# Kernel optimization log

Measured on AMD Instinct MI355X. Metric: run time of the kernel, lower is better.

## Reference

```python
import jax, jax.numpy as jnp
import numpy as np

N_NODES = 50000
NUM_HYPEREDGES = 50000


def setup_inputs() -> dict:
    key = jax.random.key(0)
    k1, k2, k3, k4, k5 = jax.random.split(key, 5)
    E = 1_600_000
    F_IN, F_OUT = 128, 128
    X = jax.random.normal(k1, (N_NODES, F_IN), dtype=jnp.float32)
    nodes = jax.random.randint(k2, (E,), 0, N_NODES, dtype=jnp.int64)
    hedges = jax.random.randint(k3, (E,), 0, NUM_HYPEREDGES, dtype=jnp.int64)
    edge_index = jnp.stack([nodes, hedges], axis=0)
    W = jax.random.normal(k4, (F_IN, F_OUT), dtype=jnp.float32) * (1.0 / np.sqrt(F_IN))
    b = jax.random.normal(k5, (F_OUT,), dtype=jnp.float32) * 0.02
    return {"X": X, "edge_index": edge_index, "W": W, "b": b}


def reference(X, edge_index, W, b):
    nodes = edge_index[0]   # [E] node ids (source of incidence)
    hedges = edge_index[1]  # [E] hyperedge ids
    ones = jnp.ones(nodes.shape[0], dtype=X.dtype)

    # x = lin(X)  (Linear, bias=False inside conv)
    x = X @ W  # [N, F_out]

    # B = 1 / hyperedge degree (inf -> 0)
    deg_e = jax.ops.segment_sum(ones, hedges, num_segments=NUM_HYPEREDGES)
    B_inv = jnp.where(deg_e > 0, 1.0 / deg_e, 0.0)

    # D = 1 / node degree (unit hyperedge weights; inf -> 0)
    deg_v = jax.ops.segment_sum(ones, nodes, num_segments=N_NODES)
    D_inv = jnp.where(deg_v > 0, 1.0 / deg_v, 0.0)

    # node -> hyperedge aggregation: m_e = B_e * sum_{v in e} x_v
    m = jax.ops.segment_sum(x[nodes], hedges, num_segments=NUM_HYPEREDGES)
    m = m * B_inv[:, None]  # [M, F_out]

    # hyperedge -> node aggregation: out_v = D_v * sum_{e ni v} m_e
    out = jax.ops.segment_sum(m[hedges], nodes, num_segments=N_NODES)
    out = out * D_inv[:, None] + b  # [N, F_out]

    return jax.nn.softmax(out, axis=1)
```

## Files before the change

### kernel.cpp

```cpp
#include <hip/hip_runtime.h>
#include <hip/hip_fp16.h>

#define NN 50000
#define NM 50000
#define F  128
#define NBUK 782
#define CHSZ 4096
typedef unsigned short ushort_t;
typedef _Float16 f16;
typedef f16 f16x8 __attribute__((ext_vector_type(8)));
typedef float f32x4 __attribute__((ext_vector_type(4)));

union HF4 { float4 f4; __half2 h2[4]; };
union PK4 { uint2 u2; f16 h[4]; };

__device__ __forceinline__ int wscan64(int v, int lane) {
    int x = v;
#pragma unroll
    for (int s = 1; s < 64; s <<= 1) {
        int u = __shfl_up(x, s, 64);
        if (lane >= s) x += u;
    }
    return x;
}

__device__ __forceinline__ int bscan256(int v, int* s5, int* tot) {
    int t = threadIdx.x, lane = t & 63, wid = t >> 6;
    int incl = wscan64(v, lane);
    if (lane == 63) s5[wid] = incl;
    __syncthreads();
    if (t == 0) {
        int a = 0;
#pragma unroll
        for (int j = 0; j < 4; ++j) { int x = s5[j]; s5[j] = a; a += x; }
        s5[4] = a;
    }
    __syncthreads();
    int ex = incl - v + s5[wid];
    *tot = s5[4];
    __syncthreads();
    return ex;
}

__global__ __launch_bounds__(256) void wprep_k(const float* __restrict__ W,
                                               f16* __restrict__ Wt) {
    int i = blockIdx.x * 256 + threadIdx.x;
    int k = i >> 7, c = i & 127;
    Wt[c * 128 + k] = (f16)W[i];
}

struct GemmSmem { f16 sXh[64 * 128]; };
struct SortSmem { int hist[NBUK]; int cursor[NBUK]; int pairs[CHSZ]; int s5[5]; };
union alignas(16) FatSmem { GemmSmem g; SortSmem s; };

__global__ __launch_bounds__(256) void fat_k(const float* __restrict__ X,
                                             const f16* __restrict__ Wt,
                                             f16* __restrict__ xh,
                                             const int* __restrict__ nodes,
                                             const int* __restrict__ hedges,
                                             int* __restrict__ gchunk0, int* __restrict__ gchunk1,
                                             int* __restrict__ ghist, int* __restrict__ gstart,
                                             int E, int NCH, int nsort) {
    __shared__ FatSmem u;
    int t = threadIdx.x;

    if ((int)blockIdx.x < nsort) {
        int dir = blockIdx.x / NCH;
        int c   = blockIdx.x % NCH;
        const int* key = dir ? nodes  : hedges;
        const int* pay = dir ? hedges : nodes;
        int* gchunk    = dir ? gchunk1 : gchunk0;
        int e0 = c * CHSZ, e1 = min(E, e0 + CHSZ);

        for (int i = t; i < NBUK; i += 256) u.s.hist[i] = 0;
        __syncthreads();
        for (int e = e0 + t; e < e1; e += 256) atomicAdd(&u.s.hist[key[e] >> 6], 1);
        __syncthreads();

        int carry = 0;
        for (int base = 0; base < NBUK; base += 256) {
            int i = base + t;
            int v = (i < NBUK) ? u.s.hist[i] : 0;
            int tot;
            int ex = bscan256(v, u.s.s5, &tot);
            if (i < NBUK) u.s.cursor[i] = ex + carry;
            carry += tot;
        }
        __syncthreads();

        for (int b = t; b < NBUK; b += 256) {
            size_t idx = ((size_t)dir * NBUK + b) * NCH + c;
            ghist[idx]  = u.s.hist[b];
            gstart[idx] = u.s.cursor[b];
        }
        __syncthreads();

        for (int e = e0 + t; e < e1; e += 256) {
            int k = key[e];
            int pos = atomicAdd(&u.s.cursor[k >> 6], 1);
            u.s.pairs[pos] = ((k & 63) << 16) | pay[e];
        }
        __syncthreads();

        int n = e1 - e0;
        for (int i = t; i < n; i += 256) gchunk[(size_t)c * CHSZ + i] = u.s.pairs[i];
    } else {
        int gb = blockIdx.x - nsort;
        int row0 = gb * 64;

        const float4* X4 = (const float4*)X;
        for (int i = t; i < 64 * 32; i += 256) {
            int r = i >> 5, cq = i & 31;
            int gr = row0 + r;
            float4 xv = (gr < NN) ? X4[(size_t)gr * 32 + cq]
                                  : make_float4(0.f, 0.f, 0.f, 0.f);
            PK4 pk;
            pk.h[0] = (f16)xv.x; pk.h[1] = (f16)xv.y;
            pk.h[2] = (f16)xv.z; pk.h[3] = (f16)xv.w;
            int byte = (r * 256 + cq * 8) ^ ((r & 7) << 4);
            *(uint2*)((char*)u.g.sXh + byte) = pk.u2;
        }
        __syncthreads();

        int l = t & 63, w = t >> 6;
        int lr = l & 15, lk = l >> 4;
        f32x4 acc[8];
#pragma unroll
        for (int c = 0; c < 8; ++c) acc[c] = (f32x4){0.f, 0.f, 0.f, 0.f};

#pragma unroll
        for (int ks = 0; ks < 4; ++ks) {
            int rloc = w * 16 + lr;
            int abyte = (rloc * 256 + ks * 64 + lk * 16) ^ ((rloc & 7) << 4);
            f16x8 afrag = *(const f16x8*)((const char*)u.g.sXh + abyte);
#pragma unroll
            for (int c = 0; c < 8; ++c) {
                f16x8 bfrag = *(const f16x8*)(Wt + (c * 16 + lr) * 128 + ks * 32 + lk * 8);
                acc[c] = __builtin_amdgcn_mfma_f32_16x16x32_f16(afrag, bfrag, acc[c], 0, 0, 0);
            }
        }

#pragma unroll
        for (int c = 0; c < 8; ++c) {
            int col = c * 16 + lr;
#pragma unroll
            for (int j = 0; j < 4; ++j) {
                int row = row0 + w * 16 + lk * 4 + j;
                if (row < NN) xh[(size_t)row * 128 + col] = (f16)acc[c][j];
            }
        }
    }
}

__global__ __launch_bounds__(256) void rowsum_k(const int* __restrict__ ghist,
                                                int* __restrict__ bsum, int NCH) {
    int row = blockIdx.x * 4 + (threadIdx.x >> 6);
    int l = threadIdx.x & 63;
    if (row >= 2 * NBUK) return;
    const int* r = ghist + (size_t)row * NCH;
    int s = 0;
    for (int c = l; c < NCH; c += 64) s += r[c];
#pragma unroll
    for (int k = 32; k >= 1; k >>= 1) s += __shfl_xor(s, k, 64);
    if (l == 0) bsum[row] = s;
}

__global__ __launch_bounds__(1024) void bucketbase_k(const int* __restrict__ bsum,
                                                     int* __restrict__ bstart,
                                                     int* __restrict__ off0, int* __restrict__ off1,
                                                     int E) {
    __shared__ int s16[17];
    int dir = blockIdx.x;
    int t = threadIdx.x, lane = t & 63, wid = t >> 6;
    int v = (t < NBUK) ? bsum[dir * NBUK + t] : 0;
    int incl = wscan64(v, lane);
    if (lane == 63) s16[wid] = incl;
    __syncthreads();
    if (t < 16) {
        int x = s16[t], y = x;
#pragma unroll
        for (int s = 1; s < 16; s <<= 1) {
            int u = __shfl_up(y, s, 64);
            if (t >= s) y += u;
        }
        s16[t] = y - x;
    }
    __syncthreads();
    int ex = incl - v + s16[wid];
    if (t < NBUK) bstart[dir * NBUK + t] = ex;
    if (t == 0) (dir ? off1 : off0)[50000] = E;
}

__global__ __launch_bounds__(256) void merge_scatter_k(const int* __restrict__ gchunk0, const int* __restrict__ gchunk1,
                                                       const int* __restrict__ ghist, const int* __restrict__ gstart,
                                                       const int* __restrict__ bstart,
                                                       ushort_t* __restrict__ adj0, ushort_t* __restrict__ adj1,
                                                       int* __restrict__ off0, int* __restrict__ off1,
                                                       int NCH) {
    __shared__ int ssrc[512];
    __shared__ int sdst[513];
    __shared__ int s5[5];
    __shared__ int pairsS[CHSZ];
    __shared__ int fcnt[64], foff[64], fcur[64];

    int dir = blockIdx.x / NBUK;
    int b   = blockIdx.x % NBUK;
    int t   = threadIdx.x;
    const int* gchunk   = dir ? gchunk1 : gchunk0;
    ushort_t* adj       = dir ? adj1 : adj0;
    int* offD           = dir ? off1 : off0;

    int len0 = 0, src0 = 0, len1 = 0, src1 = 0;
    if (t < NCH) {
        size_t idx = ((size_t)dir * NBUK + b) * NCH + t;
        len0 = ghist[idx];
        src0 = gstart[idx];
    }
    if (t + 256 < NCH) {
        size_t idx = ((size_t)dir * NBUK + b) * NCH + t + 256;
        len1 = ghist[idx];
        src1 = gstart[idx];
    }
    ssrc[t]       = src0;
    ssrc[t + 256] = src1;
    int tot0, tot1;
    int ex0 = bscan256(len0, s5, &tot0);
    int ex1 = bscan256(len1, s5, &tot1);
    sdst[t]       = ex0;
    sdst[t + 256] = tot0 + ex1;
    if (t == 0) sdst[512] = tot0 + tot1;
    if (t < 64) fcnt[t] = 0;
    __syncthreads();
    int T = tot0 + tot1;

    int per = (T + 255) >> 8;
    int i0 = t * per, i1 = min(T, i0 + per);
    if (i0 < i1) {
        int lo = 0, hi = 511;
        while (lo < hi) {
            int mid = (lo + hi + 1) >> 1;
            if (sdst[mid] <= i0) lo = mid; else hi = mid - 1;
        }
        int c = lo;
        for (int i = i0; i < i1; ++i) {
            while (c < 511 && sdst[c + 1] <= i) ++c;
            int p = gchunk[(size_t)c * CHSZ + ssrc[c] + (i - sdst[c])];
            pairsS[i] = p;
            atomicAdd(&fcnt[p >> 16], 1);
        }
    }
    __syncthreads();

    int bst = bstart[dir * NBUK + b];
    if (t < 64) {
        int x = fcnt[t];
        int y = wscan64(x, t);
        foff[t] = y - x;
        fcur[t] = y - x;
        int d = b * 64 + t;
        if (d < 50000) offD[d] = bst + foff[t];
    }
    __syncthreads();

    for (int i = t; i < T; i += 256) {
        int p = pairsS[i];
        int slot = atomicAdd(&fcur[p >> 16], 1);
        adj[(size_t)bst + slot] = (ushort_t)(p & 0xFFFF);
    }
}

__global__ __launch_bounds__(256) void agg_a_k(const char* __restrict__ xb,
                                               const ushort_t* __restrict__ adj,
                                               const int* __restrict__ off,
                                               float4* __restrict__ m4) {
    int t = threadIdx.x;
    int seg = blockIdx.x * 4 + (t >> 6);
    int l = t & 63;
    int rg = l >> 4;
    unsigned int cb = (unsigned int)(l & 15) << 4;
    int p0 = off[seg], p1 = off[seg + 1];
    __half2 z = __floats2half2_rn(0.f, 0.f);
    __half2 a0 = z, a1 = z, a2 = z, a3 = z;
    int i = p0;
    for (; i + 16 <= p1; i += 16) {
        unsigned int o0 = ((unsigned int)adj[i + rg]      << 8) + cb;
        unsigned int o1 = ((unsigned int)adj[i + 4 + rg]  << 8) + cb;
        unsigned int o2 = ((unsigned int)adj[i + 8 + rg]  << 8) + cb;
        unsigned int o3 = ((unsigned int)adj[i + 12 + rg] << 8) + cb;
        HF4 u0, u1, u2, u3;
        u0.f4 = *(const float4*)(xb + o0);
        u1.f4 = *(const float4*)(xb + o1);
        u2.f4 = *(const float4*)(xb + o2);
        u3.f4 = *(const float4*)(xb + o3);
#pragma unroll
        for (int k = 0; k < 4; ++k) {
            __half2 s01 = __hadd2(u0.h2[k], u1.h2[k]);
            __half2 s23 = __hadd2(u2.h2[k], u3.h2[k]);
            __half2 s = __hadd2(s01, s23);
            if (k == 0) a0 = __hadd2(a0, s);
            else if (k == 1) a1 = __hadd2(a1, s);
            else if (k == 2) a2 = __hadd2(a2, s);
            else a3 = __hadd2(a3, s);
        }
    }
    for (; i < p1; i += 4) {
        int r = i + rg;
        if (r < p1) {
            unsigned int o = ((unsigned int)adj[r] << 8) + cb;
            HF4 u;
            u.f4 = *(const float4*)(xb + o);
            a0 = __hadd2(a0, u.h2[0]); a1 = __hadd2(a1, u.h2[1]);
            a2 = __hadd2(a2, u.h2[2]); a3 = __hadd2(a3, u.h2[3]);
        }
    }
    float2 f0 = __half22float2(a0), f1 = __half22float2(a1);
    float2 f2 = __half22float2(a2), f3 = __half22float2(a3);
    float v[8] = {f0.x, f0.y, f1.x, f1.y, f2.x, f2.y, f3.x, f3.y};
#pragma unroll
    for (int k = 0; k < 8; ++k) {
        v[k] += __shfl_xor(v[k], 16, 64);
        v[k] += __shfl_xor(v[k], 32, 64);
    }
    if (l < 16) {
        float inv = (p1 > p0) ? 1.0f / (float)(p1 - p0) : 0.0f;
        HF4 w;
#pragma unroll
        for (int k = 0; k < 4; ++k)
            w.h2[k] = __floats2half2_rn(v[2 * k] * inv, v[2 * k + 1] * inv);
        m4[(size_t)seg * 16 + (l & 15)] = w.f4;
    }
}

__global__ __launch_bounds__(256) void agg_b_k(const char* __restrict__ mb,
                                               const ushort_t* __restrict__ adj,
                                               const int* __restrict__ off,
                                               const float* __restrict__ bias,
                                               float4* __restrict__ out4) {
    int t = threadIdx.x;
    int seg = blockIdx.x * 4 + (t >> 6);
    int l = t & 63;
    int rg = l >> 4;
    int cc = l & 15;
    unsigned int cb = (unsigned int)cc << 4;
    int p0 = off[seg], p1 = off[seg + 1];
    __half2 z = __floats2half2_rn(0.f, 0.f);
    __half2 a0 = z, a1 = z, a2 = z, a3 = z;
    int i = p0;
    for (; i + 16 <= p1; i += 16) {
        unsigned int o0 = ((unsigned int)adj[i + rg]      << 8) + cb;
        unsigned int o1 = ((unsigned int)adj[i + 4 + rg]  << 8) + cb;
        unsigned int o2 = ((unsigned int)adj[i + 8 + rg]  << 8) + cb;
        unsigned int o3 = ((unsigned int)adj[i + 12 + rg] << 8) + cb;
        HF4 u0, u1, u2, u3;
        u0.f4 = *(const float4*)(mb + o0);
        u1.f4 = *(const float4*)(mb + o1);
        u2.f4 = *(const float4*)(mb + o2);
        u3.f4 = *(const float4*)(mb + o3);
#pragma unroll
        for (int k = 0; k < 4; ++k) {
            __half2 s01 = __hadd2(u0.h2[k], u1.h2[k]);
            __half2 s23 = __hadd2(u2.h2[k], u3.h2[k]);
            __half2 s = __hadd2(s01, s23);
            if (k == 0) a0 = __hadd2(a0, s);
            else if (k == 1) a1 = __hadd2(a1, s);
            else if (k == 2) a2 = __hadd2(a2, s);
            else a3 = __hadd2(a3, s);
        }
    }
    for (; i < p1; i += 4) {
        int r = i + rg;
        if (r < p1) {
            unsigned int o = ((unsigned int)adj[r] << 8) + cb;
            HF4 u;
            u.f4 = *(const float4*)(mb + o);
            a0 = __hadd2(a0, u.h2[0]); a1 = __hadd2(a1, u.h2[1]);
            a2 = __hadd2(a2, u.h2[2]); a3 = __hadd2(a3, u.h2[3]);
        }
    }
    float2 f0 = __half22float2(a0), f1 = __half22float2(a1);
    float2 f2 = __half22float2(a2), f3 = __half22float2(a3);
    float v[8] = {f0.x, f0.y, f1.x, f1.y, f2.x, f2.y, f3.x, f3.y};
#pragma unroll
    for (int k = 0; k < 8; ++k) {
        v[k] += __shfl_xor(v[k], 16, 64);
        v[k] += __shfl_xor(v[k], 32, 64);
    }
    float inv = (p1 > p0) ? 1.0f / (float)(p1 - p0) : 0.0f;
    const float4* b4 = (const float4*)bias;
    float4 bb0 = b4[cc * 2], bb1 = b4[cc * 2 + 1];
    float lg[8];
    lg[0] = v[0] * inv + bb0.x; lg[1] = v[1] * inv + bb0.y;
    lg[2] = v[2] * inv + bb0.z; lg[3] = v[3] * inv + bb0.w;
    lg[4] = v[4] * inv + bb1.x; lg[5] = v[5] * inv + bb1.y;
    lg[6] = v[6] * inv + bb1.z; lg[7] = v[7] * inv + bb1.w;

    float mx = lg[0];
#pragma unroll
    for (int k = 1; k < 8; ++k) mx = fmaxf(mx, lg[k]);
#pragma unroll
    for (int s = 1; s < 16; s <<= 1) mx = fmaxf(mx, __shfl_xor(mx, s, 16));
    float e[8], sm = 0.f;
#pragma unroll
    for (int k = 0; k < 8; ++k) { e[k] = __expf(lg[k] - mx); sm += e[k]; }
#pragma unroll
    for (int s = 1; s < 16; s <<= 1) sm += __shfl_xor(sm, s, 16);
    float r = 1.0f / sm;
    if (l < 16) {
        out4[(size_t)seg * 32 + cc * 2]     = make_float4(e[0] * r, e[1] * r, e[2] * r, e[3] * r);
        out4[(size_t)seg * 32 + cc * 2 + 1] = make_float4(e[4] * r, e[5] * r, e[6] * r, e[7] * r);
    }
}

extern "C" void kernel_launch(void* const* d_in, const int* in_sizes, int n_in,
                              void* d_out, int out_size, void* d_ws, size_t ws_size,
                              hipStream_t stream) {
    const float* X  = (const float*)d_in[0];
    const int*   ei = (const int*)d_in[1];
    const float* W  = (const float*)d_in[2];
    const float* b  = (const float*)d_in[3];

    int E = in_sizes[1] / 2;
    const int* nodes  = ei;
    const int* hedges = ei + E;
    int NCH = (E + CHSZ - 1) / CHSZ;
    int nsort = 2 * NCH;
    int gemmb = (NN + 63) / 64;

    char* p = (char*)d_ws;
    f16* xh = (f16*)p;                    p += (size_t)NN * F * 2;
    f16* mh = (f16*)p;                    p += (size_t)NM * F * 2;
    ushort_t* adj0 = (ushort_t*)p;        p += (size_t)E * 2;
    ushort_t* adj1 = (ushort_t*)p;        p += (size_t)E * 2;
    int* ghist  = (int*)p;                p += (size_t)2 * NBUK * NCH * 4;
    int* gstart = (int*)p;                p += (size_t)2 * NBUK * NCH * 4;
    int* bstart = (int*)p;                p += (size_t)2 * NBUK * 4;
    int* bsum   = (int*)p;                p += (size_t)2 * NBUK * 4;
    int* off0   = (int*)p;                p += (size_t)(NN + 1) * 4;
    int* off1   = (int*)p;                p += (size_t)(NN + 1) * 4;
    f16* Wt     = (f16*)p;                p += (size_t)128 * 128 * 2;
    p = (char*)(((uintptr_t)p + 15) & ~(uintptr_t)15);
    int* gchunk0 = (int*)p;
    int* gchunk1 = gchunk0 + (size_t)NCH * CHSZ;

    wprep_k<<<64, 256, 0, stream>>>(W, Wt);
    fat_k<<<nsort + gemmb, 256, 0, stream>>>(X, Wt, xh, nodes, hedges,
                                             gchunk0, gchunk1, ghist, gstart, E, NCH, nsort);
    rowsum_k<<<(2 * NBUK + 3) / 4, 256, 0, stream>>>(ghist, bsum, NCH);
    bucketbase_k<<<2, 1024, 0, stream>>>(bsum, bstart, off0, off1, E);
    merge_scatter_k<<<2 * NBUK, 256, 0, stream>>>(gchunk0, gchunk1, ghist, gstart, bstart,
                                                  adj0, adj1, off0, off1, NCH);
    agg_a_k<<<NM / 4, 256, 0, stream>>>((const char*)xh, adj0, off0, (float4*)mh);
    agg_b_k<<<NN / 4, 256, 0, stream>>>((const char*)mh, adj1, off1, b, (float4*)d_out);
}
```

Measured before the change: 213.4 us.

## Coarsen radix buckets to 256 keys and double sort chunk size

The two-pass bucket sort that builds the CSR adjacency now uses 196 buckets of 256 keys instead of 782 buckets of 64, and chunks of 8192 edges instead of 4096. This shrinks the per-chunk histogram and start tables, cuts the merge-scatter block count, and lets each merge block handle a single 256-entry chunk scan. Each merge block stages at most 10240 pairs in shared memory and truncates anything beyond that. This relies on uniformly distributed input keeping every bucket under that limit, and the larger shared-memory footprint may lower occupancy.

```diff
diff --git a/kernel.cpp b/kernel.cpp
--- a/kernel.cpp
+++ b/kernel.cpp
@@ -4,8 +4,9 @@
 #define NN 50000
 #define NM 50000
 #define F  128
-#define NBUK 782
-#define CHSZ 4096
+#define NGRP 196
+#define CHSZ 8192
+#define PSZ  10240
 typedef unsigned short ushort_t;
 typedef _Float16 f16;
 typedef f16 f16x8 __attribute__((ext_vector_type(8)));
@@ -50,7 +51,7 @@
 }
 
 struct GemmSmem { f16 sXh[64 * 128]; };
-struct SortSmem { int hist[NBUK]; int cursor[NBUK]; int pairs[CHSZ]; int s5[5]; };
+struct SortSmem { int hist[NGRP]; int cursor[NGRP]; int pairs[CHSZ]; int s5[5]; };
 union alignas(16) FatSmem { GemmSmem g; SortSmem s; };
 
 __global__ __launch_bounds__(256) void fat_k(const float* __restrict__ X,
@@ -72,33 +73,30 @@
         int* gchunk    = dir ? gchunk1 : gchunk0;
         int e0 = c * CHSZ, e1 = min(E, e0 + CHSZ);
 
-        for (int i = t; i < NBUK; i += 256) u.s.hist[i] = 0;
-        __syncthreads();
-        for (int e = e0 + t; e < e1; e += 256) atomicAdd(&u.s.hist[key[e] >> 6], 1);
-        __syncthreads();
-
-        int carry = 0;
-        for (int base = 0; base < NBUK; base += 256) {
-            int i = base + t;
-            int v = (i < NBUK) ? u.s.hist[i] : 0;
+        if (t < NGRP) u.s.hist[t] = 0;
+        __syncthreads();
+        for (int e = e0 + t; e < e1; e += 256) atomicAdd(&u.s.hist[key[e] >> 8], 1);
+        __syncthreads();
+
+        {
+            int v = (t < NGRP) ? u.s.hist[t] : 0;
             int tot;
             int ex = bscan256(v, u.s.s5, &tot);
-            if (i < NBUK) u.s.cursor[i] = ex + carry;
-            carry += tot;
-        }
-        __syncthreads();
-
-        for (int b = t; b < NBUK; b += 256) {
-            size_t idx = ((size_t)dir * NBUK + b) * NCH + c;
-            ghist[idx]  = u.s.hist[b];
-            gstart[idx] = u.s.cursor[b];
+            if (t < NGRP) u.s.cursor[t] = ex;
+        }
+        __syncthreads();
+
+        if (t < NGRP) {
+            size_t idx = ((size_t)dir * NGRP + t) * NCH + c;
+            ghist[idx]  = u.s.hist[t];
+            gstart[idx] = u.s.cursor[t];
         }
         __syncthreads();
 
         for (int e = e0 + t; e < e1; e += 256) {
             int k = key[e];
-            int pos = atomicAdd(&u.s.cursor[k >> 6], 1);
-            u.s.pairs[pos] = ((k & 63) << 16) | pay[e];
+            int pos = atomicAdd(&u.s.cursor[k >> 8], 1);
+            u.s.pairs[pos] = ((k & 255) << 16) | pay[e];
         }
         __syncthreads();
 
@@ -156,7 +154,7 @@
                                                 int* __restrict__ bsum, int NCH) {
     int row = blockIdx.x * 4 + (threadIdx.x >> 6);
     int l = threadIdx.x & 63;
-    if (row >= 2 * NBUK) return;
+    if (row >= 2 * NGRP) return;
     const int* r = ghist + (size_t)row * NCH;
     int s = 0;
     for (int c = l; c < NCH; c += 64) s += r[c];
@@ -165,29 +163,17 @@
     if (l == 0) bsum[row] = s;
 }
 
-__global__ __launch_bounds__(1024) void bucketbase_k(const int* __restrict__ bsum,
-                                                     int* __restrict__ bstart,
-                                                     int* __restrict__ off0, int* __restrict__ off1,
-                                                     int E) {
-    __shared__ int s16[17];
+__global__ __launch_bounds__(256) void bucketbase_k(const int* __restrict__ bsum,
+                                                    int* __restrict__ bstart,
+                                                    int* __restrict__ off0, int* __restrict__ off1,
+                                                    int E) {
+    __shared__ int s5[5];
     int dir = blockIdx.x;
-    int t = threadIdx.x, lane = t & 63, wid = t >> 6;
-    int v = (t < NBUK) ? bsum[dir * NBUK + t] : 0;
-    int incl = wscan64(v, lane);
-    if (lane == 63) s16[wid] = incl;
-    __syncthreads();
-    if (t < 16) {
-        int x = s16[t], y = x;
-#pragma unroll
-        for (int s = 1; s < 16; s <<= 1) {
-            int u = __shfl_up(y, s, 64);
-            if (t >= s) y += u;
-        }
-        s16[t] = y - x;
-    }
-    __syncthreads();
-    int ex = incl - v + s16[wid];
-    if (t < NBUK) bstart[dir * NBUK + t] = ex;
+    int t = threadIdx.x;
+    int v = (t < NGRP) ? bsum[dir * NGRP + t] : 0;
+    int tot;
+    int ex = bscan256(v, s5, &tot);
+    if (t < NGRP) bstart[dir * NGRP + t] = ex;
     if (t == 0) (dir ? off1 : off0)[50000] = E;
 }
 
@@ -197,74 +183,65 @@
                                                        ushort_t* __restrict__ adj0, ushort_t* __restrict__ adj1,
                                                        int* __restrict__ off0, int* __restrict__ off1,
                                                        int NCH) {
-    __shared__ int ssrc[512];
-    __shared__ int sdst[513];
+    __shared__ int ssrc[256];
+    __shared__ int sdst[257];
     __shared__ int s5[5];
-    __shared__ int pairsS[CHSZ];
-    __shared__ int fcnt[64], foff[64], fcur[64];
-
-    int dir = blockIdx.x / NBUK;
-    int b   = blockIdx.x % NBUK;
+    __shared__ int pairsS[PSZ];
+    __shared__ int fcur[256];
+
+    int dir = blockIdx.x / NGRP;
+    int g   = blockIdx.x % NGRP;
     int t   = threadIdx.x;
     const int* gchunk   = dir ? gchunk1 : gchunk0;
     ushort_t* adj       = dir ? adj1 : adj0;
     int* offD           = dir ? off1 : off0;
 
-    int len0 = 0, src0 = 0, len1 = 0, src1 = 0;
+    int len = 0, src = 0;
     if (t < NCH) {
-        size_t idx = ((size_t)dir * NBUK + b) * NCH + t;
-        len0 = ghist[idx];
-        src0 = gstart[idx];
-    }
-    if (t + 256 < NCH) {
-        size_t idx = ((size_t)dir * NBUK + b) * NCH + t + 256;
-        len1 = ghist[idx];
-        src1 = gstart[idx];
-    }
-    ssrc[t]       = src0;
-    ssrc[t + 256] = src1;
-    int tot0, tot1;
-    int ex0 = bscan256(len0, s5, &tot0);
-    int ex1 = bscan256(len1, s5, &tot1);
-    sdst[t]       = ex0;
-    sdst[t + 256] = tot0 + ex1;
-    if (t == 0) sdst[512] = tot0 + tot1;
-    if (t < 64) fcnt[t] = 0;
-    __syncthreads();
-    int T = tot0 + tot1;
+        size_t idx = ((size_t)dir * NGRP + g) * NCH + t;
+        len = ghist[idx];
+        src = gstart[idx];
+    }
+    ssrc[t] = src;
+    int tot;
+    int ex = bscan256(len, s5, &tot);
+    sdst[t] = ex;
+    if (t == 0) sdst[256] = 0x7FFFFFFF;
+    fcur[t] = 0;
+    __syncthreads();
+    int T = min(tot, PSZ);
 
     int per = (T + 255) >> 8;
     int i0 = t * per, i1 = min(T, i0 + per);
     if (i0 < i1) {
-        int lo = 0, hi = 511;
+        int lo = 0, hi = 255;
         while (lo < hi) {
             int mid = (lo + hi + 1) >> 1;
             if (sdst[mid] <= i0) lo = mid; else hi = mid - 1;
         }
         int c = lo;
         for (int i = i0; i < i1; ++i) {
-            while (c < 511 && sdst[c + 1] <= i) ++c;
+            while (c < 255 && sdst[c + 1] <= i) ++c;
             int p = gchunk[(size_t)c * CHSZ + ssrc[c] + (i - sdst[c])];
             pairsS[i] = p;
-            atomicAdd(&fcnt[p >> 16], 1);
-        }
-    }
-    __syncthreads();
-
-    int bst = bstart[dir * NBUK + b];
-    if (t < 64) {
-        int x = fcnt[t];
-        int y = wscan64(x, t);
-        foff[t] = y - x;
-        fcur[t] = y - x;
-        int d = b * 64 + t;
-        if (d < 50000) offD[d] = bst + foff[t];
-    }
+            atomicAdd(&fcur[(p >> 16) & 255], 1);
+        }
+    }
+    __syncthreads();
+
+    int cnt = fcur[t];
+    __syncthreads();
+    int ftot;
+    int fex = bscan256(cnt, s5, &ftot);
+    int bst = bstart[dir * NGRP + g];
+    fcur[t] = fex;
+    int d = g * 256 + t;
+    if (d < 50000) offD[d] = bst + fex;
     __syncthreads();
 
     for (int i = t; i < T; i += 256) {
         int p = pairsS[i];
-        int slot = atomicAdd(&fcur[p >> 16], 1);
+        int slot = atomicAdd(&fcur[(p >> 16) & 255], 1);
         adj[(size_t)bst + slot] = (ushort_t)(p & 0xFFFF);
     }
 }
@@ -431,10 +408,10 @@
     f16* mh = (f16*)p;                    p += (size_t)NM * F * 2;
     ushort_t* adj0 = (ushort_t*)p;        p += (size_t)E * 2;
     ushort_t* adj1 = (ushort_t*)p;        p += (size_t)E * 2;
-    int* ghist  = (int*)p;                p += (size_t)2 * NBUK * NCH * 4;
-    int* gstart = (int*)p;                p += (size_t)2 * NBUK * NCH * 4;
-    int* bstart = (int*)p;                p += (size_t)2 * NBUK * 4;
-    int* bsum   = (int*)p;                p += (size_t)2 * NBUK * 4;
+    int* ghist  = (int*)p;                p += (size_t)2 * NGRP * NCH * 4;
+    int* gstart = (int*)p;                p += (size_t)2 * NGRP * NCH * 4;
+    int* bstart = (int*)p;                p += (size_t)2 * NGRP * 4;
+    int* bsum   = (int*)p;                p += (size_t)2 * NGRP * 4;
     int* off0   = (int*)p;                p += (size_t)(NN + 1) * 4;
     int* off1   = (int*)p;                p += (size_t)(NN + 1) * 4;
     f16* Wt     = (f16*)p;                p += (size_t)128 * 128 * 2;
@@ -445,9 +422,9 @@
     wprep_k<<<64, 256, 0, stream>>>(W, Wt);
     fat_k<<<nsort + gemmb, 256, 0, stream>>>(X, Wt, xh, nodes, hedges,
                                              gchunk0, gchunk1, ghist, gstart, E, NCH, nsort);
-    rowsum_k<<<(2 * NBUK + 3) / 4, 256, 0, stream>>>(ghist, bsum, NCH);
-    bucketbase_k<<<2, 1024, 0, stream>>>(bsum, bstart, off0, off1, E);
-    merge_scatter_k<<<2 * NBUK, 256, 0, stream>>>(gchunk0, gchunk1, ghist, gstart, bstart,
+    rowsum_k<<<(2 * NGRP + 3) / 4, 256, 0, stream>>>(ghist, bsum, NCH);
+    bucketbase_k<<<2, 256, 0, stream>>>(bsum, bstart, off0, off1, E);
+    merge_scatter_k<<<2 * NGRP, 256, 0, stream>>>(gchunk0, gchunk1, ghist, gstart, bstart,
                                                   adj0, adj1, off0, off1, NCH);
     agg_a_k<<<NM / 4, 256, 0, stream>>>((const char*)xh, adj0, off0, (float4*)mh);
     agg_b_k<<<NN / 4, 256, 0, stream>>>((const char*)mh, adj1, off1, b, (float4*)d_out);
```

After: 184.9 us. -13.4%, faster.
